# Optimization experiments

Hardware: AMD Instinct MI355X
Metric: run time of the kernel (lower is better)

Reference implementation:

```python
import jax, jax.numpy as jnp
import numpy as np

SPARSITY = 0.1  # fraction of entries kept (set to 1)


def _subnet(scores, k):
    # Mirrors GetSubnet.forward: full sort of flattened |scores|, zero the
    # lowest j = int((1-k)*n) ranks, set the rest to 1 (ties broken by sort order).
    flat = scores.ravel()
    n = flat.size
    j = int((1.0 - k) * n)  # static python int
    order = jnp.argsort(flat)  # ascending
    out = jnp.zeros((n,), dtype=scores.dtype).at[order[j:]].set(1)
    return out.reshape(scores.shape)


def setup_inputs() -> dict:
    key = jax.random.key(0)
    kA, kB = jax.random.split(key)
    # kaiming_uniform_(a=sqrt(5)) => U(-bound, bound), bound = sqrt(6/((1+5)*fan_in)) = 1/sqrt(fan_in)
    A_shape = (1024, 16384)
    B_shape = (16384, 1024)
    bA = 1.0 / np.sqrt(A_shape[1])
    bB = 1.0 / np.sqrt(B_shape[1])
    lora_A_mask = jax.random.uniform(kA, A_shape, jnp.float32, -bA, bA)
    lora_B_mask = jax.random.uniform(kB, B_shape, jnp.float32, -bB, bB)
    return {"lora_A_mask": lora_A_mask, "lora_B_mask": lora_B_mask}


def reference(lora_A_mask, lora_B_mask):
    mask_A = _subnet(jnp.abs(lora_A_mask), SPARSITY)
    mask_B = _subnet(jnp.abs(lora_B_mask), SPARSITY)
    return (mask_A, mask_B)
```

## Files before the change

kernel.cpp:

```cpp
#include <hip/hip_runtime.h>
#include <stdint.h>

#define OFF_H1     0u
#define OFF_H2     2048u
#define OFF_H3     4096u
#define OFF_PREFIX 6144u
#define OFF_RANK   6145u
#define OFF_T      6146u
#define OFF_C      6147u
#define OFF_CNT    6148u
#define OFF_BCNT   6656u
#define OFF_BUF    7168u
#define CAP        8192u
#define MAT_WORDS  (7168u + 2u * CAP)
#define SUB        4
#define NB2        512
#define SEGCAP     16384u

__global__ void init_k(uint32_t* __restrict__ ws) {
  uint32_t i = blockIdx.x * blockDim.x + threadIdx.x;
  if (i < 6656u) { ws[i] = 0u; ws[MAT_WORDS + i] = 0u; }
}

__global__ void hist1_k(const float* __restrict__ A, const float* __restrict__ B,
                        uint32_t* __restrict__ ws, int nvec) {
  const int m = blockIdx.y;
  const float4* __restrict__ src = (const float4*)(m == 0 ? A : B);
  uint32_t* W = ws + (size_t)m * MAT_WORDS;
  __shared__ uint32_t h[2048 * SUB];
  for (int i = threadIdx.x; i < 2048 * SUB; i += blockDim.x) h[i] = 0u;
  __syncthreads();
  const uint32_t sub = threadIdx.x & (SUB - 1);
  int idx0 = blockIdx.x * blockDim.x + threadIdx.x;
  int stride = gridDim.x * blockDim.x;
  for (int i = idx0; i < nvec; i += stride) {
    float4 f = src[i];
    const float v[4] = {f.x, f.y, f.z, f.w};
#pragma unroll
    for (int c = 0; c < 4; c++) {
      uint32_t u = __float_as_uint(v[c]) & 0x7fffffffu;
      atomicAdd(&h[(u >> 21) * SUB + sub], 1u);
    }
  }
  __syncthreads();
  uint32_t* gh = W + OFF_H1;
  for (int b = threadIdx.x; b < 2048; b += blockDim.x) {
    uint32_t s = 0u;
#pragma unroll
    for (int k = 0; k < SUB; k++) s += h[b * SUB + k];
    if (s) atomicAdd(&gh[b], s);
  }
}

__global__ void hist2_k(const float* __restrict__ A, const float* __restrict__ B,
                        uint32_t* __restrict__ ws, uint32_t* __restrict__ outbuf,
                        int nvec) {
  const int m = blockIdx.y;
  const float4* __restrict__ src = (const float4*)(m == 0 ? A : B);
  uint32_t* W = ws + (size_t)m * MAT_WORDS;
  uint32_t* seg = outbuf + (size_t)m * 16777216u + (size_t)blockIdx.x * (SEGCAP * 2u);
  __shared__ uint32_t h[2048 * SUB];
  __shared__ uint32_t segn;
  for (int i = threadIdx.x; i < 2048 * SUB; i += blockDim.x) h[i] = 0u;
  if (threadIdx.x == 0) segn = 0u;
  uint32_t prefix = W[OFF_PREFIX];
  __syncthreads();
  const uint32_t sub = threadIdx.x & (SUB - 1);
  int idx0 = blockIdx.x * blockDim.x + threadIdx.x;
  int stride = gridDim.x * blockDim.x;
  for (int i = idx0; i < nvec; i += stride) {
    float4 f = src[i];
    const float v[4] = {f.x, f.y, f.z, f.w};
#pragma unroll
    for (int c = 0; c < 4; c++) {
      uint32_t u = __float_as_uint(v[c]) & 0x7fffffffu;
      if ((u >> 21) == (prefix >> 21)) {
        atomicAdd(&h[((u >> 10) & 2047u) * SUB + sub], 1u);
        uint32_t s = atomicAdd(&segn, 1u);
        if (s < SEGCAP) { seg[2u * s] = (uint32_t)i * 4u + (uint32_t)c; seg[2u * s + 1u] = u; }
      }
    }
  }
  __syncthreads();
  uint32_t* gh = W + OFF_H2;
  for (int b = threadIdx.x; b < 2048; b += blockDim.x) {
    uint32_t s = 0u;
#pragma unroll
    for (int k = 0; k < SUB; k++) s += h[b * SUB + k];
    if (s) atomicAdd(&gh[b], s);
  }
  if (threadIdx.x == 0) {
    uint32_t s = segn; if (s > SEGCAP) s = SEGCAP;
    W[OFF_BCNT + blockIdx.x] = s;
  }
}

template <int PASS>
__global__ void scan_k(uint32_t* __restrict__ ws, uint32_t j) {
  const int m = blockIdx.x;
  uint32_t* W = ws + (size_t)m * MAT_WORDS;
  const uint32_t* hist = W + (PASS == 1 ? OFF_H1 : OFF_H2);
  __shared__ uint32_t h[2048];
  __shared__ uint32_t ps[256];
  const int t = threadIdx.x;
  uint32_t r = (PASS == 1) ? j : W[OFF_RANK];
  uint32_t prefix = (PASS == 1) ? 0u : W[OFF_PREFIX];
  uint32_t s = 0u;
  for (int k = 0; k < 8; k++) {
    int b = t * 8 + k;
    uint32_t v = hist[b];
    h[b] = v;
    s += v;
  }
  ps[t] = s;
  __syncthreads();
  for (int off = 1; off < 256; off <<= 1) {
    uint32_t v = (t >= off) ? ps[t - off] : 0u;
    __syncthreads();
    ps[t] += v;
    __syncthreads();
  }
  uint32_t base = (t == 0) ? 0u : ps[t - 1];
  for (int k = 0; k < 8; k++) {
    int b = t * 8 + k;
    uint32_t c = h[b];
    if (r >= base && r < base + c) {
      if (PASS == 1) W[OFF_PREFIX] = (uint32_t)b << 21;
      else           W[OFF_PREFIX] = prefix | ((uint32_t)b << 10);
      W[OFF_RANK] = r - base;
    }
    base += c;
  }
}

__global__ void pass3_k(uint32_t* __restrict__ ws, const uint32_t* __restrict__ outbuf) {
  const int m = blockIdx.y;
  uint32_t* W = ws + (size_t)m * MAT_WORDS;
  const uint32_t* seg = outbuf + (size_t)m * 16777216u + (size_t)blockIdx.x * (SEGCAP * 2u);
  __shared__ uint32_t h[1024];
  for (int i = threadIdx.x; i < 1024; i += blockDim.x) h[i] = 0u;
  uint32_t n = W[OFF_BCNT + blockIdx.x];
  uint32_t prefix = W[OFF_PREFIX];
  __syncthreads();
  for (uint32_t e = threadIdx.x; e < n; e += blockDim.x) {
    uint32_t idx = seg[2u * e];
    uint32_t u   = seg[2u * e + 1u];
    if ((u >> 10) == (prefix >> 10)) {
      atomicAdd(&h[u & 1023u], 1u);
      uint32_t slot = atomicAdd(&W[OFF_CNT], 1u);
      if (slot < CAP) { W[OFF_BUF + 2u * slot] = idx; W[OFF_BUF + 2u * slot + 1u] = u; }
    }
  }
  __syncthreads();
  for (int b = threadIdx.x; b < 1024; b += blockDim.x)
    if (h[b]) atomicAdd(&W[OFF_H3 + b], h[b]);
}

__global__ void scan3tie_k(uint32_t* __restrict__ ws) {
  const int m = blockIdx.x;
  uint32_t* W = ws + (size_t)m * MAT_WORDS;
  __shared__ uint32_t h[1024];
  __shared__ uint32_t ps[256];
  __shared__ uint32_t sT, sTarget;
  __shared__ uint32_t tie_idx[1024];
  __shared__ uint32_t tie_n;
  const int t = threadIdx.x;
  uint32_t r = W[OFF_RANK];
  uint32_t prefix = W[OFF_PREFIX];
  uint32_t cnt = W[OFF_CNT]; if (cnt > CAP) cnt = CAP;
  if (t == 0) tie_n = 0u;
  uint32_t s = 0u;
  for (int k = 0; k < 4; k++) {
    int b = t * 4 + k;
    uint32_t v = W[OFF_H3 + b];
    h[b] = v;
    s += v;
  }
  ps[t] = s;
  __syncthreads();
  for (int off = 1; off < 256; off <<= 1) {
    uint32_t v = (t >= off) ? ps[t - off] : 0u;
    __syncthreads();
    ps[t] += v;
    __syncthreads();
  }
  uint32_t base = (t == 0) ? 0u : ps[t - 1];
  for (int k = 0; k < 4; k++) {
    int b = t * 4 + k;
    uint32_t c = h[b];
    if (r >= base && r < base + c) { sT = prefix | (uint32_t)b; sTarget = r - base; }
    base += c;
  }
  __syncthreads();
  const uint32_t T = sT, target = sTarget;
  for (uint32_t c2 = t; c2 < cnt; c2 += 256u) {
    if (W[OFF_BUF + 2u * c2 + 1u] == T) {
      uint32_t slot = atomicAdd(&tie_n, 1u);
      if (slot < 1024u) tie_idx[slot] = W[OFF_BUF + 2u * c2];
    }
  }
  __syncthreads();
  uint32_t E2 = tie_n; if (E2 > 1024u) E2 = 1024u;
  for (uint32_t c2 = t; c2 < E2; c2 += 256u) {
    uint32_t xi = tie_idx[c2];
    uint32_t lt = 0u;
    for (uint32_t k2 = 0; k2 < E2; k2++) lt += (tie_idx[k2] < xi) ? 1u : 0u;
    if (lt == target) W[OFF_C] = xi;
  }
  if (t == 0) W[OFF_T] = T;
}

__global__ void mask_k(const float* __restrict__ A, const float* __restrict__ B,
                       float* __restrict__ out, const uint32_t* __restrict__ ws,
                       int nvec, int n) {
  const int m = blockIdx.y;
  const float4* __restrict__ src = (const float4*)(m == 0 ? A : B);
  float4* __restrict__ dst = (float4*)(out + (size_t)m * (size_t)n);
  const uint32_t* W = ws + (size_t)m * MAT_WORDS;
  const uint32_t T = W[OFF_T];
  const uint32_t C = W[OFF_C];
  int idx0 = blockIdx.x * blockDim.x + threadIdx.x;
  int stride = gridDim.x * blockDim.x;
  for (int i = idx0; i < nvec; i += stride) {
    float4 f = src[i];
    const float v[4] = {f.x, f.y, f.z, f.w};
    float r[4];
#pragma unroll
    for (int c = 0; c < 4; c++) {
      uint32_t u = __float_as_uint(v[c]) & 0x7fffffffu;
      uint32_t idx = (uint32_t)i * 4u + (uint32_t)c;
      r[c] = (u > T || (u == T && idx >= C)) ? 1.0f : 0.0f;
    }
    dst[i] = make_float4(r[0], r[1], r[2], r[3]);
  }
}

extern "C" void kernel_launch(void* const* d_in, const int* in_sizes, int n_in,
                              void* d_out, int out_size, void* d_ws, size_t ws_size,
                              hipStream_t stream) {
  const float* A = (const float*)d_in[0];
  const float* B = (const float*)d_in[1];
  float* out = (float*)d_out;
  uint32_t* ws = (uint32_t*)d_ws;
  uint32_t* outbuf = (uint32_t*)d_out;
  const int n = in_sizes[0];
  const int nvec = n / 4;
  const uint32_t j = (uint32_t)((1.0 - 0.1) * (double)n);

  init_k<<<(6656 + 255) / 256, 256, 0, stream>>>(ws);
  hist1_k<<<dim3(1024, 2), 256, 0, stream>>>(A, B, ws, nvec);
  scan_k<1><<<2, 256, 0, stream>>>(ws, j);
  hist2_k<<<dim3(NB2, 2), 256, 0, stream>>>(A, B, ws, outbuf, nvec);
  scan_k<2><<<2, 256, 0, stream>>>(ws, j);
  pass3_k<<<dim3(NB2, 2), 256, 0, stream>>>(ws, outbuf);
  scan3tie_k<<<2, 256, 0, stream>>>(ws);
  mask_k<<<dim3(2048, 2), 256, 0, stream>>>(A, B, out, ws, nvec, n);
}
```

Before: 334.9 us.

## Sample-based pivot prefilter to compact candidates, replacing second full-input histogram pass

Adds a sampling kernel that histograms 65536 strided elements to pick a conservative lower bound G that should lie below the top-10% threshold. The first full pass then histograms only elements at or above G and compacts them (index, value) into a buffer in the output region. The second and third radix passes read only this compacted buffer instead of re-reading the full inputs. This removes one full read of both 64MB matrices, at the cost of per-iteration block barriers and global atomics for compaction. Correctness depends on the sample bound holding, since elements below G are dropped.

Measured after the change: 651.8 us. 94.6% more time.

```diff
diff --git a/kernel.cpp b/kernel.cpp
--- a/kernel.cpp
+++ b/kernel.cpp
@@ -1,116 +1,145 @@
 #include <hip/hip_runtime.h>
 #include <stdint.h>
 
-#define OFF_H1     0u
-#define OFF_H2     2048u
-#define OFF_H3     4096u
-#define OFF_PREFIX 6144u
-#define OFF_RANK   6145u
-#define OFF_T      6146u
-#define OFF_C      6147u
-#define OFF_CNT    6148u
-#define OFF_BCNT   6656u
-#define OFF_BUF    7168u
-#define CAP        8192u
-#define MAT_WORDS  (7168u + 2u * CAP)
-#define SUB        4
-#define NB2        512
-#define SEGCAP     16384u
+#define OFF_SH     0u
+#define OFF_H1     16384u
+#define OFF_H2     18432u
+#define OFF_H3     20480u
+#define OFF_G      21504u
+#define OFF_CNT    21505u
+#define OFF_PREFIX 21506u
+#define OFF_RANK   21507u
+#define OFF_T      21508u
+#define OFF_C      21509u
+#define OFF_TCNT   21510u
+#define OFF_TBUF   21512u
+#define TCAP       8192u
+#define MAT_WORDS  (21512u + 2u * TCAP)
+#define INIT_WORDS 21512u
+#define CAPBUF     8388608u
 
 __global__ void init_k(uint32_t* __restrict__ ws) {
   uint32_t i = blockIdx.x * blockDim.x + threadIdx.x;
-  if (i < 6656u) { ws[i] = 0u; ws[MAT_WORDS + i] = 0u; }
-}
-
-__global__ void hist1_k(const float* __restrict__ A, const float* __restrict__ B,
-                        uint32_t* __restrict__ ws, int nvec) {
+  if (i < INIT_WORDS) { ws[i] = 0u; ws[MAT_WORDS + i] = 0u; }
+}
+
+__global__ void sample_k(const float* __restrict__ A, const float* __restrict__ B,
+                         uint32_t* __restrict__ ws, int nvec) {
   const int m = blockIdx.y;
   const float4* __restrict__ src = (const float4*)(m == 0 ? A : B);
   uint32_t* W = ws + (size_t)m * MAT_WORDS;
-  __shared__ uint32_t h[2048 * SUB];
-  for (int i = threadIdx.x; i < 2048 * SUB; i += blockDim.x) h[i] = 0u;
-  __syncthreads();
-  const uint32_t sub = threadIdx.x & (SUB - 1);
+  __shared__ uint32_t sh[16384];
+  for (int i = threadIdx.x; i < 16384; i += blockDim.x) sh[i] = 0u;
+  __syncthreads();
+  const int w = threadIdx.x >> 6, lane = threadIdx.x & 63;
+  const int cstride = nvec / 256;
+  for (int it = 0; it < 4; it++) {
+    int chunk = blockIdx.x * 16 + it * 4 + w;
+    int fi = chunk * cstride + lane;
+    if (fi < nvec) {
+      float4 f = src[fi];
+      const float v[4] = {f.x, f.y, f.z, f.w};
+#pragma unroll
+      for (int c = 0; c < 4; c++) {
+        uint32_t u = __float_as_uint(v[c]) & 0x7fffffffu;
+        atomicAdd(&sh[u >> 17], 1u);
+      }
+    }
+  }
+  __syncthreads();
+  for (int b = threadIdx.x; b < 16384; b += blockDim.x)
+    if (sh[b]) atomicAdd(&W[OFF_SH + b], sh[b]);
+}
+
+__global__ void scanG_k(uint32_t* __restrict__ ws, uint32_t need) {
+  const int m = blockIdx.x;
+  uint32_t* W = ws + (size_t)m * MAT_WORDS;
+  __shared__ uint32_t ps[256];
+  __shared__ int sbest;
+  const int t = threadIdx.x;
+  if (t == 0) sbest = -1;
+  uint32_t sum = 0u;
+  for (int k = 0; k < 64; k++) sum += W[OFF_SH + t * 64 + k];
+  ps[t] = sum;
+  __syncthreads();
+  for (int off = 1; off < 256; off <<= 1) {
+    uint32_t v = (t >= off) ? ps[t - off] : 0u;
+    __syncthreads();
+    ps[t] += v;
+    __syncthreads();
+  }
+  uint32_t total = ps[255];
+  uint32_t cum = ps[t] - sum;
+  int best = -1;
+  for (int k = 0; k < 64; k++) {
+    int b = t * 64 + k;
+    if (total - cum >= need) best = b;
+    cum += W[OFF_SH + b];
+  }
+  if (best >= 0) atomicMax(&sbest, best);
+  __syncthreads();
+  if (t == 0) W[OFF_G] = (sbest >= 0) ? ((uint32_t)sbest << 17) : 0u;
+}
+
+__global__ void pass1_k(const float* __restrict__ A, const float* __restrict__ B,
+                        uint32_t* __restrict__ ws, uint32_t* __restrict__ outbuf,
+                        int nvec) {
+  const int m = blockIdx.y;
+  const float4* __restrict__ src = (const float4*)(m == 0 ? A : B);
+  uint32_t* W = ws + (size_t)m * MAT_WORDS;
+  uint2* __restrict__ buf = (uint2*)(outbuf + (size_t)m * 16777216u);
+  __shared__ uint32_t h[2048 * 4];
+  __shared__ uint32_t lcnt, lbase;
+  for (int i = threadIdx.x; i < 2048 * 4; i += blockDim.x) h[i] = 0u;
+  const uint32_t G = W[OFF_G];
+  __syncthreads();
+  const uint32_t sub = threadIdx.x & 3u;
   int idx0 = blockIdx.x * blockDim.x + threadIdx.x;
   int stride = gridDim.x * blockDim.x;
   for (int i = idx0; i < nvec; i += stride) {
     float4 f = src[i];
     const float v[4] = {f.x, f.y, f.z, f.w};
+    uint32_t cu[4], ci[4], tc = 0u;
 #pragma unroll
     for (int c = 0; c < 4; c++) {
       uint32_t u = __float_as_uint(v[c]) & 0x7fffffffu;
-      atomicAdd(&h[(u >> 21) * SUB + sub], 1u);
-    }
-  }
-  __syncthreads();
-  uint32_t* gh = W + OFF_H1;
+      if (u >= G) {
+        cu[tc] = u; ci[tc] = (uint32_t)i * 4u + (uint32_t)c; tc++;
+        atomicAdd(&h[(u >> 21) * 4u + sub], 1u);
+      }
+    }
+    if (threadIdx.x == 0) lcnt = 0u;
+    __syncthreads();
+    uint32_t off = tc ? atomicAdd(&lcnt, tc) : 0u;
+    __syncthreads();
+    if (threadIdx.x == 0) lbase = lcnt ? atomicAdd(&W[OFF_CNT], lcnt) : 0u;
+    __syncthreads();
+    uint32_t base = lbase + off;
+    for (uint32_t k = 0; k < tc; k++) {
+      uint32_t s = base + k;
+      if (s < CAPBUF) buf[s] = make_uint2(ci[k], cu[k]);
+    }
+  }
+  __syncthreads();
   for (int b = threadIdx.x; b < 2048; b += blockDim.x) {
-    uint32_t s = 0u;
-#pragma unroll
-    for (int k = 0; k < SUB; k++) s += h[b * SUB + k];
-    if (s) atomicAdd(&gh[b], s);
-  }
-}
-
-__global__ void hist2_k(const float* __restrict__ A, const float* __restrict__ B,
-                        uint32_t* __restrict__ ws, uint32_t* __restrict__ outbuf,
-                        int nvec) {
-  const int m = blockIdx.y;
-  const float4* __restrict__ src = (const float4*)(m == 0 ? A : B);
-  uint32_t* W = ws + (size_t)m * MAT_WORDS;
-  uint32_t* seg = outbuf + (size_t)m * 16777216u + (size_t)blockIdx.x * (SEGCAP * 2u);
-  __shared__ uint32_t h[2048 * SUB];
-  __shared__ uint32_t segn;
-  for (int i = threadIdx.x; i < 2048 * SUB; i += blockDim.x) h[i] = 0u;
-  if (threadIdx.x == 0) segn = 0u;
-  uint32_t prefix = W[OFF_PREFIX];
-  __syncthreads();
-  const uint32_t sub = threadIdx.x & (SUB - 1);
-  int idx0 = blockIdx.x * blockDim.x + threadIdx.x;
-  int stride = gridDim.x * blockDim.x;
-  for (int i = idx0; i < nvec; i += stride) {
-    float4 f = src[i];
-    const float v[4] = {f.x, f.y, f.z, f.w};
-#pragma unroll
-    for (int c = 0; c < 4; c++) {
-      uint32_t u = __float_as_uint(v[c]) & 0x7fffffffu;
-      if ((u >> 21) == (prefix >> 21)) {
-        atomicAdd(&h[((u >> 10) & 2047u) * SUB + sub], 1u);
-        uint32_t s = atomicAdd(&segn, 1u);
-        if (s < SEGCAP) { seg[2u * s] = (uint32_t)i * 4u + (uint32_t)c; seg[2u * s + 1u] = u; }
-      }
-    }
-  }
-  __syncthreads();
-  uint32_t* gh = W + OFF_H2;
-  for (int b = threadIdx.x; b < 2048; b += blockDim.x) {
-    uint32_t s = 0u;
-#pragma unroll
-    for (int k = 0; k < SUB; k++) s += h[b * SUB + k];
-    if (s) atomicAdd(&gh[b], s);
-  }
-  if (threadIdx.x == 0) {
-    uint32_t s = segn; if (s > SEGCAP) s = SEGCAP;
-    W[OFF_BCNT + blockIdx.x] = s;
-  }
-}
-
-template <int PASS>
-__global__ void scan_k(uint32_t* __restrict__ ws, uint32_t j) {
+    uint32_t s = h[b * 4] + h[b * 4 + 1] + h[b * 4 + 2] + h[b * 4 + 3];
+    if (s) atomicAdd(&W[OFF_H1 + b], s);
+  }
+}
+
+__global__ void scan1_k(uint32_t* __restrict__ ws, uint32_t keep) {
   const int m = blockIdx.x;
   uint32_t* W = ws + (size_t)m * MAT_WORDS;
-  const uint32_t* hist = W + (PASS == 1 ? OFF_H1 : OFF_H2);
   __shared__ uint32_t h[2048];
   __shared__ uint32_t ps[256];
   const int t = threadIdx.x;
-  uint32_t r = (PASS == 1) ? j : W[OFF_RANK];
-  uint32_t prefix = (PASS == 1) ? 0u : W[OFF_PREFIX];
+  uint32_t cnt = W[OFF_CNT]; if (cnt > CAPBUF) cnt = CAPBUF;
+  uint32_t r = cnt - keep;
   uint32_t s = 0u;
   for (int k = 0; k < 8; k++) {
     int b = t * 8 + k;
-    uint32_t v = hist[b];
-    h[b] = v;
-    s += v;
+    uint32_t v = W[OFF_H1 + b];
+    h[b] = v; s += v;
   }
   ps[t] = s;
   __syncthreads();
@@ -125,30 +154,85 @@
     int b = t * 8 + k;
     uint32_t c = h[b];
     if (r >= base && r < base + c) {
-      if (PASS == 1) W[OFF_PREFIX] = (uint32_t)b << 21;
-      else           W[OFF_PREFIX] = prefix | ((uint32_t)b << 10);
-      W[OFF_RANK] = r - base;
+      W[OFF_PREFIX] = (uint32_t)b << 21;
+      W[OFF_RANK]   = r - base;
     }
     base += c;
   }
 }
 
-__global__ void pass3_k(uint32_t* __restrict__ ws, const uint32_t* __restrict__ outbuf) {
-  const int m = blockIdx.y;
-  uint32_t* W = ws + (size_t)m * MAT_WORDS;
-  const uint32_t* seg = outbuf + (size_t)m * 16777216u + (size_t)blockIdx.x * (SEGCAP * 2u);
+__global__ void hist2b_k(uint32_t* __restrict__ ws, const uint32_t* __restrict__ outbuf) {
+  const int m = blockIdx.y;
+  uint32_t* W = ws + (size_t)m * MAT_WORDS;
+  const uint2* __restrict__ buf = (const uint2*)(outbuf + (size_t)m * 16777216u);
+  __shared__ uint32_t h[2048 * 4];
+  for (int i = threadIdx.x; i < 2048 * 4; i += blockDim.x) h[i] = 0u;
+  uint32_t cnt = W[OFF_CNT]; if (cnt > CAPBUF) cnt = CAPBUF;
+  uint32_t p21 = W[OFF_PREFIX] >> 21;
+  __syncthreads();
+  const uint32_t sub = threadIdx.x & 3u;
+  for (uint32_t e = blockIdx.x * blockDim.x + threadIdx.x; e < cnt;
+       e += gridDim.x * blockDim.x) {
+    uint2 v = buf[e];
+    if ((v.y >> 21) == p21) atomicAdd(&h[((v.y >> 10) & 2047u) * 4u + sub], 1u);
+  }
+  __syncthreads();
+  for (int b = threadIdx.x; b < 2048; b += blockDim.x) {
+    uint32_t s = h[b * 4] + h[b * 4 + 1] + h[b * 4 + 2] + h[b * 4 + 3];
+    if (s) atomicAdd(&W[OFF_H2 + b], s);
+  }
+}
+
+__global__ void scan2_k(uint32_t* __restrict__ ws) {
+  const int m = blockIdx.x;
+  uint32_t* W = ws + (size_t)m * MAT_WORDS;
+  __shared__ uint32_t h[2048];
+  __shared__ uint32_t ps[256];
+  const int t = threadIdx.x;
+  uint32_t r = W[OFF_RANK];
+  uint32_t prefix = W[OFF_PREFIX];
+  uint32_t s = 0u;
+  for (int k = 0; k < 8; k++) {
+    int b = t * 8 + k;
+    uint32_t v = W[OFF_H2 + b];
+    h[b] = v; s += v;
+  }
+  ps[t] = s;
+  __syncthreads();
+  for (int off = 1; off < 256; off <<= 1) {
+    uint32_t v = (t >= off) ? ps[t - off] : 0u;
+    __syncthreads();
+    ps[t] += v;
+    __syncthreads();
+  }
+  uint32_t base = (t == 0) ? 0u : ps[t - 1];
+  for (int k = 0; k < 8; k++) {
+    int b = t * 8 + k;
+    uint32_t c = h[b];
+    if (r >= base && r < base + c) {
+      W[OFF_PREFIX] = prefix | ((uint32_t)b << 10);
+      W[OFF_RANK]   = r - base;
+    }
+    base += c;
+  }
+}
+
+__global__ void pass3b_k(uint32_t* __restrict__ ws, const uint32_t* __restrict__ outbuf) {
+  const int m = blockIdx.y;
+  uint32_t* W = ws + (size_t)m * MAT_WORDS;
+  const uint2* __restrict__ buf = (const uint2*)(outbuf + (size_t)m * 16777216u);
   __shared__ uint32_t h[1024];
   for (int i = threadIdx.x; i < 1024; i += blockDim.x) h[i] = 0u;
-  uint32_t n = W[OFF_BCNT + blockIdx.x];
-  uint32_t prefix = W[OFF_PREFIX];
-  __syncthreads();
-  for (uint32_t e = threadIdx.x; e < n; e += blockDim.x) {
-    uint32_t idx = seg[2u * e];
-    uint32_t u   = seg[2u * e + 1u];
-    if ((u >> 10) == (prefix >> 10)) {
-      atomicAdd(&h[u & 1023u], 1u);
-      uint32_t slot = atomicAdd(&W[OFF_CNT], 1u);
-      if (slot < CAP) { W[OFF_BUF + 2u * slot] = idx; W[OFF_BUF + 2u * slot + 1u] = u; }
+  uint32_t cnt = W[OFF_CNT]; if (cnt > CAPBUF) cnt = CAPBUF;
+  uint32_t p10 = W[OFF_PREFIX] >> 10;
+  __syncthreads();
+  for (uint32_t e = blockIdx.x * blockDim.x + threadIdx.x; e < cnt;
+       e += gridDim.x * blockDim.x) {
+    uint2 v = buf[e];
+    if ((v.y >> 10) == p10) {
+      atomicAdd(&h[v.y & 1023u], 1u);
+      uint32_t slot = atomicAdd(&W[OFF_TCNT], 1u);
+      if (slot < TCAP) { W[OFF_TBUF + 2u * slot] = v.x; W[OFF_TBUF + 2u * slot + 1u] = v.y; }
     }
   }
   __syncthreads();
@@ -167,14 +251,13 @@
   const int t = threadIdx.x;
   uint32_t r = W[OFF_RANK];
   uint32_t prefix = W[OFF_PREFIX];
-  uint32_t cnt = W[OFF_CNT]; if (cnt > CAP) cnt = CAP;
+  uint32_t cnt = W[OFF_TCNT]; if (cnt > TCAP) cnt = TCAP;
   if (t == 0) tie_n = 0u;
   uint32_t s = 0u;
   for (int k = 0; k < 4; k++) {
     int b = t * 4 + k;
     uint32_t v = W[OFF_H3 + b];
-    h[b] = v;
-    s += v;
+    h[b] = v; s += v;
   }
   ps[t] = s;
   __syncthreads();
@@ -194,9 +277,9 @@
   __syncthreads();
   const uint32_t T = sT, target = sTarget;
   for (uint32_t c2 = t; c2 < cnt; c2 += 256u) {
-    if (W[OFF_BUF + 2u * c2 + 1u] == T) {
+    if (W[OFF_TBUF + 2u * c2 + 1u] == T) {
       uint32_t slot = atomicAdd(&tie_n, 1u);
-      if (slot < 1024u) tie_idx[slot] = W[OFF_BUF + 2u * c2];
+      if (slot < 1024u) tie_idx[slot] = W[OFF_TBUF + 2u * c2];
     }
   }
   __syncthreads();
@@ -246,13 +329,18 @@
   const int n = in_sizes[0];
   const int nvec = n / 4;
   const uint32_t j = (uint32_t)((1.0 - 0.1) * (double)n);
-
-  init_k<<<(6656 + 255) / 256, 256, 0, stream>>>(ws);
-  hist1_k<<<dim3(1024, 2), 256, 0, stream>>>(A, B, ws, nvec);
-  scan_k<1><<<2, 256, 0, stream>>>(ws, j);
-  hist2_k<<<dim3(NB2, 2), 256, 0, stream>>>(A, B, ws, outbuf, nvec);
-  scan_k<2><<<2, 256, 0, stream>>>(ws, j);
-  pass3_k<<<dim3(NB2, 2), 256, 0, stream>>>(ws, outbuf);
+  const uint32_t keep = (uint32_t)n - j;
+  const uint32_t samples = 65536u;
+  const uint32_t need = (13u * samples) / 100u;
+
+  init_k<<<(INIT_WORDS + 255) / 256, 256, 0, stream>>>(ws);
+  sample_k<<<dim3(16, 2), 256, 0, stream>>>(A, B, ws, nvec);
+  scanG_k<<<2, 256, 0, stream>>>(ws, need);
+  pass1_k<<<dim3(1024, 2), 256, 0, stream>>>(A, B, ws, outbuf, nvec);
+  scan1_k<<<2, 256, 0, stream>>>(ws, keep);
+  hist2b_k<<<dim3(128, 2), 256, 0, stream>>>(ws, outbuf);
+  scan2_k<<<2, 256, 0, stream>>>(ws);
+  pass3b_k<<<dim3(128, 2), 256, 0, stream>>>(ws, outbuf);
   scan3tie_k<<<2, 256, 0, stream>>>(ws);
   mask_k<<<dim3(2048, 2), 256, 0, stream>>>(A, B, out, ws, nvec, n);
 }
```
